# Optimization experiments

Measured on AMD Instinct MI355X. Metric: run time of the kernel, lower is better.

The kernel has to match this reference:

```python
import jax, jax.numpy as jnp
import numpy as np
from jax import lax

_F1 = np.array([1., 3., 3., 1.], dtype=np.float32)
_F1 = _F1 / _F1.sum()
F2D = jnp.asarray(np.outer(_F1, _F1))  # [4,4] normalized FIR filter
LRELU_GAIN = float(np.sqrt(2.0))


def _upfirdn2d_up(x, up, pad0, pad1, gain):
    # zero-insertion upsample + pad + FIR filter (VALID depthwise conv)
    B, C, H, W = x.shape
    if up > 1:
        x = jnp.zeros((B, C, H, up, W, up), x.dtype).at[:, :, :, 0, :, 0].set(x)
        x = x.reshape(B, C, H * up, W * up)
    x = jnp.pad(x, ((0, 0), (0, 0), (pad0, pad1), (pad0, pad1)))
    k = jnp.broadcast_to((F2D * gain).astype(x.dtype), (C, 1, 4, 4))
    return lax.conv_general_dilated(x, k, (1, 1), 'VALID', feature_group_count=C)


def _affine(w, aw, ab):
    # FullyConnectedLayer: weight_gain = 1/sqrt(in_features), bias_init handled in setup
    return w @ aw.T * (1.0 / np.sqrt(aw.shape[1])) + ab


def _mod_conv(x, weight, styles, up):
    # fused modulated conv2d with demodulation, batch-as-groups trick
    B = x.shape[0]
    O, I, kh, kw = weight.shape
    w = weight[None] * styles[:, None, :, None, None]          # [B,O,I,kh,kw]
    d = lax.rsqrt(jnp.sum(jnp.square(w), axis=(2, 3, 4)) + 1e-8)  # [B,O]
    w = w * d[:, :, None, None, None]
    if up == 2:
        # conv2d_resample: FIR upsample (gain=up^2), then true conv (flipped weight)
        # padding=1, fw=4, up=2 -> px0 = 1 + (4+2-1)//2 = 3, px1 = 1 + (4-2)//2 = 2
        x = _upfirdn2d_up(x, 2, 3, 2, 4.0)
        w = w[:, :, :, ::-1, ::-1]
        pad = 'VALID'
    else:
        pad = ((kh // 2, kh // 2), (kw // 2, kw // 2))
    xr = x.reshape(1, B * I, x.shape[2], x.shape[3])
    wr = w.reshape(B * O, I, kh, kw)
    y = lax.conv_general_dilated(xr, wr, (1, 1), pad, feature_group_count=B)
    return y.reshape(B, O, y.shape[2], y.shape[3])


def _lrelu_bias(x, b, clamp=256.0):
    # bias_act: lrelu(x+b) * sqrt(2), clamp
    x = x + b[None, :, None, None]
    x = jnp.where(x >= 0, x, 0.2 * x) * LRELU_GAIN
    return jnp.clip(x, -clamp, clamp)


def setup_inputs() -> dict:
    key = jax.random.key(0)
    ks = jax.random.split(key, 12)
    B, Cin, Cout, Wd, R, IC = 8, 512, 512, 512, 64, 3
    r = R // 2
    return dict(
        x=jax.random.normal(ks[0], (B, Cin, r, r), jnp.float32),
        img=jax.random.normal(ks[1], (B, IC, r, r), jnp.float32),
        ws=jax.random.normal(ks[2], (B, 3, Wd), jnp.float32),
        a0_w=jax.random.normal(ks[3], (Cin, Wd), jnp.float32),
        a0_b=jnp.ones((Cin,), jnp.float32),
        w0=jax.random.normal(ks[4], (Cout, Cin, 3, 3), jnp.float32),
        b0=jnp.zeros((Cout,), jnp.float32),
        ns0=jnp.asarray(0.1, jnp.float32),
        nc0=jax.random.normal(ks[5], (R, R), jnp.float32),
        a1_w=jax.random.normal(ks[6], (Cout, Wd), jnp.float32),
        a1_b=jnp.ones((Cout,), jnp.float32),
        w1=jax.random.normal(ks[7], (Cout, Cout, 3, 3), jnp.float32),
        b1=jnp.zeros((Cout,), jnp.float32),
        ns1=jnp.asarray(0.1, jnp.float32),
        nc1=jax.random.normal(ks[8], (R, R), jnp.float32),
        at_w=jax.random.normal(ks[9], (Cout, Wd), jnp.float32),
        at_b=jnp.ones((Cout,), jnp.float32),
        wt=jax.random.normal(ks[10], (IC, Cout), jnp.float32),
        bt=jnp.zeros((IC,), jnp.float32),
    )


def reference(x, img, ws, a0_w, a0_b, w0, b0, ns0, nc0,
              a1_w, a1_b, w1, b1, ns1, nc1, at_w, at_b, wt, bt):
    # conv0: modulated conv, up=2, const noise, lrelu bias-act with clamp
    s0 = _affine(ws[:, 0], a0_w, a0_b)
    h = _mod_conv(x, w0, s0, up=2)
    h = h + nc0[None, None] * ns0
    h = _lrelu_bias(h, b0)
    # conv1: modulated conv, up=1
    s1 = _affine(ws[:, 1], a1_w, a1_b)
    h = _mod_conv(h, w1, s1, up=1)
    h = h + nc1[None, None] * ns1
    h = _lrelu_bias(h, b1)
    # skip architecture: upsample img (upsample2d: px0=2, px1=1, gain=4)
    img_up = _upfirdn2d_up(img, 2, 2, 1, 4.0)
    # torgb: 1x1 modulated conv, no demodulation, styles scaled by weight_gain
    st = _affine(ws[:, 2], at_w, at_b) * (1.0 / np.sqrt(wt.shape[1]))
    y = jnp.einsum('bihw,bi,oi->bohw', h, st, wt)
    y = jnp.clip(y + bt[None, :, None, None], -256.0, 256.0)
    return h, img_up + y
```

## Files before the change

kernel.cpp:

```cpp
#include <hip/hip_runtime.h>
#include <stdint.h>

typedef unsigned short u16;
typedef unsigned int   u32;

#define DEVINL __device__ __forceinline__

typedef __bf16 bf16x8 __attribute__((ext_vector_type(8)));
typedef float  f32x4  __attribute__((ext_vector_type(4)));
typedef unsigned short u16x8 __attribute__((ext_vector_type(8)));

#define RSQRT512 0.044194173824159216f
#define LRELU_G  1.4142135623730951f

DEVINL u16 f2bf(float f) {
  union { float f; u32 u; } v; v.f = f;
  u32 r = v.u + 0x7fffu + ((v.u >> 16) & 1u);
  return (u16)(r >> 16);
}
DEVINL float bf2f(u16 b) {
  union { u32 u; float f; } v; v.u = ((u32)b) << 16;
  return v.f;
}

#define AS1 __attribute__((address_space(1)))
#define AS3 __attribute__((address_space(3)))
DEVINL void gload16(const void* g, void* l) {
  __builtin_amdgcn_global_load_lds((AS1 const u32*)(uintptr_t)g,
                                   (AS3 u32*)(u32)(uintptr_t)l, 16, 0, 0);
}

__global__ __launch_bounds__(256)
void style_kernel(const float* __restrict__ wsin,
                  const float* __restrict__ a0w, const float* __restrict__ a0b,
                  const float* __restrict__ a1w, const float* __restrict__ a1b,
                  const float* __restrict__ atw, const float* __restrict__ atb,
                  float* __restrict__ s_all)
{
  int wid = threadIdx.x >> 6, lane = threadIdx.x & 63;
  int idx = blockIdx.x * 4 + wid;
  int j = idx >> 12;
  int b = (idx >> 9) & 7;
  int o = idx & 511;
  const float* A  = (j == 0) ? a0w : ((j == 1) ? a1w : atw);
  const float* Ab = (j == 0) ? a0b : ((j == 1) ? a1b : atb);
  const float* wv = wsin + (b * 3 + j) * 512;
  float p = 0.f;
  #pragma unroll
  for (int m = 0; m < 512; m += 64) p += wv[m + lane] * A[(size_t)o * 512 + m + lane];
  #pragma unroll
  for (int s = 32; s; s >>= 1) p += __shfl_xor(p, s, 64);
  if (lane == 0) {
    float v = p * RSQRT512 + Ab[o];
    if (j == 2) v *= RSQRT512;
    s_all[idx] = v;
  }
}

__global__ __launch_bounds__(256)
void demod_kernel(const float* __restrict__ w, const float* __restrict__ s_j,
                  float* __restrict__ dOut)
{
  int b = blockIdx.x >> 9;
  int o = blockIdx.x & 511;
  __shared__ float s_sh[512];
  __shared__ float red[4];
  int t = threadIdx.x;
  s_sh[t]       = s_j[b * 512 + t];
  s_sh[t + 256] = s_j[b * 512 + t + 256];
  __syncthreads();
  float ssq = 0.f;
  #pragma unroll
  for (int hh = 0; hh < 2; ++hh) {
    int i = t + hh * 256;
    float si = s_sh[i];
    const float* wp = w + ((size_t)o * 512 + i) * 9;
    #pragma unroll
    for (int k = 0; k < 9; ++k) { float v = wp[k] * si; ssq += v * v; }
  }
  #pragma unroll
  for (int s = 32; s; s >>= 1) ssq += __shfl_xor(ssq, s, 64);
  if ((t & 63) == 0) red[t >> 6] = ssq;
  __syncthreads();
  if (t == 0) {
    float d = red[0] + red[1] + red[2] + red[3];
    dOut[b * 512 + o] = 1.0f / sqrtf(d + 1e-8f);
  }
}

template <int FLIP>
__global__ __launch_bounds__(256)
void wpack_kernel(const float* __restrict__ w, const float* __restrict__ s_j,
                  const float* __restrict__ dIn, u16* __restrict__ wg)
{
  int b = blockIdx.x >> 6;
  int kq = blockIdx.x & 63;
  float sv[8];
  #pragma unroll
  for (int e = 0; e < 8; ++e) sv[e] = s_j[b * 512 + kq * 8 + e];
  int t = threadIdx.x;
  #pragma unroll 1
  for (int rep = 0; rep < 2; ++rep) {
    int o = rep * 256 + t;
    float d = dIn[b * 512 + o];
    const float* wp = w + ((size_t)o * 512 + kq * 8) * 9;
    float wv[72];
    #pragma unroll
    for (int j = 0; j < 72; ++j) wv[j] = wp[j];
    #pragma unroll
    for (int tapOut = 0; tapOut < 9; ++tapOut) {
      int ksrc = FLIP ? (8 - tapOut) : tapOut;
      u16x8 g;
      #pragma unroll
      for (int e = 0; e < 8; ++e) g[e] = f2bf(wv[e * 9 + ksrc] * sv[e] * d);
      *(u16x8*)&wg[((((size_t)(b * 9 + tapOut)) * 64 + kq) * 512 + o) * 8] = g;
    }
  }
}

__global__ __launch_bounds__(256)
void upblur_kernel(const float* __restrict__ x, u16* __restrict__ xb)
{
  int b = blockIdx.x >> 6, c8 = blockIdx.x & 63;
  __shared__ float slab[8192];
  int t = threadIdx.x;
  const float* sp = x + (((size_t)(b * 512 + c8 * 8)) << 10);
  #pragma unroll
  for (int i = 0; i < 32; ++i) slab[t + i * 256] = sp[t + i * 256];
  __syncthreads();
  u16* ob = xb + ((size_t)(b * 64 + c8)) * 34848;
  #pragma unroll 1
  for (int idx = t; idx < 4356; idx += 256) {
    int p = idx / 66;
    int q = idx - p * 66;
    int m0, m1; float wy0, wy1;
    if ((p & 1) == 0) { m0 = (p >> 1) - 1; wy0 = 0.75f; m1 = p >> 1;       wy1 = 0.25f; }
    else              { m0 = (p - 3) >> 1; wy0 = 0.25f; m1 = (p - 1) >> 1; wy1 = 0.75f; }
    int n0, n1; float wx0, wx1;
    if ((q & 1) == 0) { n0 = (q >> 1) - 1; wx0 = 0.75f; n1 = q >> 1;       wx1 = 0.25f; }
    else              { n0 = (q - 3) >> 1; wx0 = 0.25f; n1 = (q - 1) >> 1; wx1 = 0.75f; }
    bool vm0 = (unsigned)m0 < 32u, vm1 = (unsigned)m1 < 32u;
    bool vn0 = (unsigned)n0 < 32u, vn1 = (unsigned)n1 < 32u;
    float w00 = (vm0 & vn0) ? wy0 * wx0 : 0.f;
    float w01 = (vm0 & vn1) ? wy0 * wx1 : 0.f;
    float w10 = (vm1 & vn0) ? wy1 * wx0 : 0.f;
    float w11 = (vm1 & vn1) ? wy1 * wx1 : 0.f;
    int i00 = ((m0 & 31) << 5) + (n0 & 31);
    int i01 = ((m0 & 31) << 5) + (n1 & 31);
    int i10 = ((m1 & 31) << 5) + (n0 & 31);
    int i11 = ((m1 & 31) << 5) + (n1 & 31);
    u16x8 g;
    #pragma unroll
    for (int e = 0; e < 8; ++e) {
      const float* se = slab + (e << 10);
      float a = w00 * se[i00] + w01 * se[i01] + w10 * se[i10] + w11 * se[i11];
      g[e] = f2bf(a);
    }
    *(u16x8*)&ob[idx * 8] = g;
  }
}

extern __shared__ u16 dynLds[];

template <int EPI>
__global__ __launch_bounds__(512, 2)
void conv8(const u16* __restrict__ xin,
           const u16* __restrict__ wg,
           const float* __restrict__ noise,
           const float* __restrict__ nsp,
           const float* __restrict__ bias,
           u16* __restrict__ hpOut,
           float* __restrict__ hOut)
{
  int blk = (blockIdx.x & 7) * 32 + (blockIdx.x >> 3);
  int b  = blk >> 5;
  int ot = (blk >> 4) & 1;
  int pt = blk & 15;
  int o0 = ot << 8;
  int y0 = pt << 2;

  int t = threadIdx.x;
  int w = t >> 6;
  int lane = t & 63;
  int gq = lane >> 4, r = lane & 15;
  int wm = w >> 2;
  int wn = w & 3;

  u16* Wb0 = dynLds;
  u16* Wb1 = dynLds + 16384;
  u16* Xb0 = dynLds + 32768;
  u16* Xb1 = dynLds + 49152;

  f32x4 acc[8][4];
  #pragma unroll
  for (int i = 0; i < 8; ++i)
    #pragma unroll
    for (int j = 0; j < 4; ++j) acc[i][j] = (f32x4){0.f, 0.f, 0.f, 0.f};

  const u16* wbB = wg + (size_t)b * 2359296;
  const u16* xbB = xin + (size_t)b * 2230272;

  auto STAGE = [&](int tile, int pb) {
    int tap = tile >> 3;
    int ck  = tile & 7;
    int dy = (tap * 171) >> 9;
    int dx = tap - dy * 3;
    u16* dW = (pb ? Wb1 : Wb0) + w * 2048;
    u16* dX = (pb ? Xb1 : Xb0) + w * 2048;
    const u16* wsrc = wbB + ((size_t)(tap * 64 + ck * 8 + w)) * 4096 + (size_t)o0 * 8;
    const u16* xsrc = xbB + ((size_t)(ck * 8 + w) * 66) * 66 * 8;
    #pragma unroll
    for (int q = 0; q < 4; ++q) {
      int row = q * 64 + lane;
      gload16(wsrc + (size_t)row * 8, dW + q * 512);
      int yy = y0 + q + dy;
      int xx = lane + dx;
      gload16(xsrc + (((size_t)yy * 66) + xx) * 8, dX + q * 512);
    }
  };

  auto TILE = [&](int pb) {
    const u16* Wp = pb ? Wb1 : Wb0;
    const u16* Xp = pb ? Xb1 : Xb0;
    const u16* A = (EPI == 0) ? Xp : Wp;
    const u16* B = (EPI == 0) ? Wp : Xp;
    bf16x8 bfr[4][2];
    #pragma unroll
    for (int fb = 0; fb < 4; ++fb)
      #pragma unroll
      for (int kk = 0; kk < 2; ++kk)
        bfr[fb][kk] = *(const bf16x8*)&B[((kk * 4 + gq) << 11) + ((wn * 64 + fb * 16 + r) << 3)];
    __builtin_amdgcn_s_setprio(1);
    #pragma unroll
    for (int fa = 0; fa < 8; ++fa) {
      int rowA = (wm * 128 + fa * 16 + r) << 3;
      bf16x8 a0 = *(const bf16x8*)&A[(gq << 11) + rowA];
      bf16x8 a1 = *(const bf16x8*)&A[((4 + gq) << 11) + rowA];
      #pragma unroll
      for (int fb = 0; fb < 4; ++fb) {
        acc[fa][fb] = __builtin_amdgcn_mfma_f32_16x16x32_bf16(a0, bfr[fb][0], acc[fa][fb], 0, 0, 0);
        acc[fa][fb] = __builtin_amdgcn_mfma_f32_16x16x32_bf16(a1, bfr[fb][1], acc[fa][fb], 0, 0, 0);
      }
    }
    __builtin_amdgcn_s_setprio(0);
  };

  STAGE(0, 0);
  STAGE(1, 1);
  asm volatile("s_waitcnt vmcnt(8)" ::: "memory");
  __builtin_amdgcn_sched_barrier(0);
  __builtin_amdgcn_s_barrier();
  __builtin_amdgcn_sched_barrier(0);

  int p = 0;
  #pragma unroll 1
  for (int tl = 0; tl < 72; ++tl) {
    TILE(p);
    __builtin_amdgcn_sched_barrier(0);
    __builtin_amdgcn_s_barrier();
    __builtin_amdgcn_sched_barrier(0);
    if (tl < 70) {
      STAGE(tl + 2, p);
      asm volatile("s_waitcnt vmcnt(8)" ::: "memory");
    } else if (tl == 70) {
      asm volatile("s_waitcnt vmcnt(0)" ::: "memory");
    }
    __builtin_amdgcn_sched_barrier(0);
    __builtin_amdgcn_s_barrier();
    __builtin_amdgcn_sched_barrier(0);
    p ^= 1;
  }
  __builtin_amdgcn_sched_barrier(0);

  float ns = nsp[0];
  if constexpr (EPI == 0) {
    #pragma unroll
    for (int fa = 0; fa < 8; ++fa) {
      #pragma unroll
      for (int fb = 0; fb < 4; ++fb) {
        int oo = o0 + wn * 64 + fb * 16 + r;
        float bo = bias[oo];
        #pragma unroll
        for (int v = 0; v < 4; ++v) {
          int px = wm * 128 + fa * 16 + gq * 4 + v;
          int pg = (pt << 8) + px;
          int y = pg >> 6, x2 = pg & 63;
          float val = acc[fa][fb][v] + noise[pg] * ns + bo;
          val = (val >= 0.f ? val : 0.2f * val) * LRELU_G;
          val = fminf(fmaxf(val, -256.f), 256.f);
          hpOut[((((size_t)b * 64 + (oo >> 3)) * 66 + (y + 1)) * 66 + (x2 + 1)) * 8 + (oo & 7)] = f2bf(val);
        }
      }
    }
  } else {
    #pragma unroll
    for (int fa = 0; fa < 8; ++fa) {
      #pragma unroll
      for (int fb = 0; fb < 4; ++fb) {
        int px = wn * 64 + fb * 16 + r;
        int pg = (pt << 8) + px;
        float nv = noise[pg] * ns;
        #pragma unroll
        for (int v = 0; v < 4; ++v) {
          int oo = o0 + wm * 128 + fa * 16 + gq * 4 + v;
          float val = acc[fa][fb][v] + nv + bias[oo];
          val = (val >= 0.f ? val : 0.2f * val) * LRELU_G;
          val = fminf(fmaxf(val, -256.f), 256.f);
          hOut[((size_t)(b * 512 + oo) << 12) + pg] = val;
        }
      }
    }
  }
}

__global__ __launch_bounds__(256)
void torgb_kernel(const float* __restrict__ h, const float* __restrict__ s_all,
                  const float* __restrict__ wt, const float* __restrict__ bt,
                  const float* __restrict__ img, float* __restrict__ out2)
{
  int b = blockIdx.x >> 4;
  int y = ((blockIdx.x & 15) << 2) + (threadIdx.x >> 6);
  int x = threadIdx.x & 63;
  __shared__ float stw[3][512];
  const float* st = s_all + 2 * 4096 + b * 512;
  for (int i = threadIdx.x; i < 512; i += 256) {
    float s = st[i];
    stw[0][i] = s * wt[i];
    stw[1][i] = s * wt[512 + i];
    stw[2][i] = s * wt[1024 + i];
  }
  __syncthreads();
  const float* hp = h + ((size_t)b * 512 << 12) + (y << 6) + x;
  float a0 = 0.f, a1 = 0.f, a2 = 0.f;
  #pragma unroll 8
  for (int i = 0; i < 512; ++i) {
    float v = hp[(size_t)i << 12];
    a0 += v * stw[0][i]; a1 += v * stw[1][i]; a2 += v * stw[2][i];
  }
  float accs[3] = {a0, a1, a2};
  int my0, my1; float wy0, wy1;
  if ((y & 1) == 0) { my0 = (y >> 1) - 1; wy0 = 0.25f; my1 = y >> 1;       wy1 = 0.75f; }
  else              { my0 = y >> 1;       wy0 = 0.75f; my1 = (y >> 1) + 1; wy1 = 0.25f; }
  int mx0, mx1; float wx0, wx1;
  if ((x & 1) == 0) { mx0 = (x >> 1) - 1; wx0 = 0.25f; mx1 = x >> 1;       wx1 = 0.75f; }
  else              { mx0 = x >> 1;       wx0 = 0.75f; mx1 = (x >> 1) + 1; wx1 = 0.25f; }
  bool vy0 = (unsigned)my0 < 32u, vy1 = (unsigned)my1 < 32u;
  bool vx0 = (unsigned)mx0 < 32u, vx1 = (unsigned)mx1 < 32u;
  #pragma unroll
  for (int o = 0; o < 3; ++o) {
    float yv = fminf(fmaxf(accs[o] + bt[o], -256.f), 256.f);
    const float* ib = img + ((size_t)(b * 3 + o) << 10);
    float iu = 0.f;
    if (vy0 & vx0) iu += wy0 * wx0 * ib[(my0 << 5) + mx0];
    if (vy0 & vx1) iu += wy0 * wx1 * ib[(my0 << 5) + mx1];
    if (vy1 & vx0) iu += wy1 * wx0 * ib[(my1 << 5) + mx0];
    if (vy1 & vx1) iu += wy1 * wx1 * ib[(my1 << 5) + mx1];
    out2[((size_t)(b * 3 + o) << 12) + (y << 6) + x] = iu + yv;
  }
}

extern "C" void kernel_launch(void* const* d_in, const int* in_sizes, int n_in,
                              void* d_out, int out_size, void* d_ws, size_t ws_size,
                              hipStream_t stream) {
  (void)in_sizes; (void)n_in; (void)out_size; (void)ws_size;
  const float* x   = (const float*)d_in[0];
  const float* img = (const float*)d_in[1];
  const float* ws_ = (const float*)d_in[2];
  const float* a0w = (const float*)d_in[3];
  const float* a0b = (const float*)d_in[4];
  const float* w0  = (const float*)d_in[5];
  const float* b0  = (const float*)d_in[6];
  const float* ns0 = (const float*)d_in[7];
  const float* nc0 = (const float*)d_in[8];
  const float* a1w = (const float*)d_in[9];
  const float* a1b = (const float*)d_in[10];
  const float* w1  = (const float*)d_in[11];
  const float* b1  = (const float*)d_in[12];
  const float* ns1 = (const float*)d_in[13];
  const float* nc1 = (const float*)d_in[14];
  const float* atw = (const float*)d_in[15];
  const float* atb = (const float*)d_in[16];
  const float* wt  = (const float*)d_in[17];
  const float* bt  = (const float*)d_in[18];

  char* wsp = (char*)d_ws;
  float* s_all = (float*)wsp;
  u16* wg0 = (u16*)(wsp + 49152);
  u16* wg1 = (u16*)(wsp + 49152 + 37748736ull);
  u16* xb  = (u16*)(wsp + 49152 + 2ull * 37748736);
  u16* hp  = (u16*)(wsp + 49152 + 2ull * 37748736 + 35684352);
  float* d0 = (float*)(wsp + 49152 + 2ull * 37748736 + 2ull * 35684352);
  float* d1 = (float*)(wsp + 49152 + 2ull * 37748736 + 2ull * 35684352 + 16384);

  float* h_out = (float*)d_out;
  float* out2  = (float*)d_out + 16777216;

  (void)hipFuncSetAttribute((const void*)conv8<0>,
                            hipFuncAttributeMaxDynamicSharedMemorySize, 131072);
  (void)hipFuncSetAttribute((const void*)conv8<1>,
                            hipFuncAttributeMaxDynamicSharedMemorySize, 131072);

  style_kernel<<<3072, 256, 0, stream>>>(ws_, a0w, a0b, a1w, a1b, atw, atb, s_all);
  demod_kernel<<<4096, 256, 0, stream>>>(w0, s_all, d0);
  demod_kernel<<<4096, 256, 0, stream>>>(w1, s_all + 4096, d1);
  wpack_kernel<1><<<512, 256, 0, stream>>>(w0, s_all, d0, wg0);
  wpack_kernel<0><<<512, 256, 0, stream>>>(w1, s_all + 4096, d1, wg1);
  upblur_kernel<<<512, 256, 0, stream>>>(x, xb);
  (void)hipMemsetAsync(hp, 0, 35684352, stream);
  conv8<0><<<256, 512, 131072, stream>>>(xb, wg0, nc0, ns0, b0, hp, nullptr);
  conv8<1><<<256, 512, 131072, stream>>>(hp, wg1, nc1, ns1, b1, nullptr, h_out);
  torgb_kernel<<<128, 256, 0, stream>>>(h_out, s_all, wt, bt, img, out2);
}
```

Before: 381.4 us.

## Split conv main loop into half-K phases interleaving staging with MFMA

Restructures the implicit-GEMM conv main loop into four phases per K tile, each covering half of K and half of the A fragments. Global-to-LDS loads for the next tile are issued in half-tile chunks between phases, with finer vmcnt waits and barriers, so memory traffic overlaps compute at a finer grain. The cost is more barriers per tile and tighter dependence on correct wait counts; the LDS layout is reorganized per half and per wave.

```diff
diff --git a/kernel.cpp b/kernel.cpp
--- a/kernel.cpp
+++ b/kernel.cpp
@@ -186,10 +186,10 @@
   int wm = w >> 2;
   int wn = w & 3;
 
-  u16* Wb0 = dynLds;
-  u16* Wb1 = dynLds + 16384;
-  u16* Xb0 = dynLds + 32768;
-  u16* Xb1 = dynLds + 49152;
+  u16* Wl = dynLds;
+  u16* Xl = dynLds + 32768;
+  const u16* Al = (EPI == 0) ? Xl : Wl;
+  const u16* Bl = (EPI == 0) ? Wl : Xl;
 
   f32x4 acc[8][4];
   #pragma unroll
@@ -200,77 +200,75 @@
   const u16* wbB = wg + (size_t)b * 2359296;
   const u16* xbB = xin + (size_t)b * 2230272;
 
-  auto STAGE = [&](int tile, int pb) {
+  int jl = w & 3;
+  int rb = w >> 2;
+
+  auto STAGEH = [&](int tile, int h) {
     int tap = tile >> 3;
     int ck  = tile & 7;
     int dy = (tap * 171) >> 9;
     int dx = tap - dy * 3;
-    u16* dW = (pb ? Wb1 : Wb0) + w * 2048;
-    u16* dX = (pb ? Xb1 : Xb0) + w * 2048;
-    const u16* wsrc = wbB + ((size_t)(tap * 64 + ck * 8 + w)) * 4096 + (size_t)o0 * 8;
-    const u16* xsrc = xbB + ((size_t)(ck * 8 + w) * 66) * 66 * 8;
-    #pragma unroll
-    for (int q = 0; q < 4; ++q) {
-      int row = q * 64 + lane;
-      gload16(wsrc + (size_t)row * 8, dW + q * 512);
-      int yy = y0 + q + dy;
-      int xx = lane + dx;
-      gload16(xsrc + (((size_t)yy * 66) + xx) * 8, dX + q * 512);
+    int jg = h * 4 + jl;
+    u32 base = (u32)((tile & 1) * 16384 + h * 8192 + jl * 2048 + rb * 1024);
+    const u16* wsrc = wbB + ((size_t)(tap * 64 + ck * 8 + jg)) * 4096
+                          + ((size_t)o0 + rb * 128) * 8;
+    const u16* xsrc = xbB + (size_t)(ck * 8 + jg) * 34848;
+    #pragma unroll
+    for (int q = 0; q < 2; ++q) {
+      gload16(wsrc + (size_t)(q * 64 + lane) * 8, Wl + base + q * 512);
+      int yy = y0 + rb * 2 + q + dy;
+      gload16(xsrc + (((size_t)yy * 66) + dx + lane) * 8, Xl + base + q * 512);
     }
   };
 
-  auto TILE = [&](int pb) {
-    const u16* Wp = pb ? Wb1 : Wb0;
-    const u16* Xp = pb ? Xb1 : Xb0;
-    const u16* A = (EPI == 0) ? Xp : Wp;
-    const u16* B = (EPI == 0) ? Wp : Xp;
-    bf16x8 bfr[4][2];
-    #pragma unroll
-    for (int fb = 0; fb < 4; ++fb)
+  auto PHASE = [&](int tb, int h, int faBase, bf16x8* bfr, bool readB,
+                   int stTile, int stH, int vm) {
+    u32 hb = (u32)(tb * 16384 + h * 8192) + ((u32)gq << 11);
+    if (readB) {
       #pragma unroll
-      for (int kk = 0; kk < 2; ++kk)
-        bfr[fb][kk] = *(const bf16x8*)&B[((kk * 4 + gq) << 11) + ((wn * 64 + fb * 16 + r) << 3)];
+      for (int fb = 0; fb < 4; ++fb)
+        bfr[fb] = *(const bf16x8*)&Bl[hb + ((wn * 64 + fb * 16 + r) << 3)];
+    }
+    bf16x8 af[4];
+    #pragma unroll
+    for (int i = 0; i < 4; ++i)
+      af[i] = *(const bf16x8*)&Al[hb + ((wm * 128 + (faBase + i) * 16 + r) << 3)];
+    if (stTile >= 0) STAGEH(stTile, stH);
+    if (vm == 4)      asm volatile("s_waitcnt vmcnt(4)" ::: "memory");
+    else if (vm == 0) asm volatile("s_waitcnt vmcnt(0)" ::: "memory");
+    __builtin_amdgcn_sched_barrier(0);
+    __builtin_amdgcn_s_barrier();
+    asm volatile("s_waitcnt lgkmcnt(0)" ::: "memory");
+    __builtin_amdgcn_sched_barrier(0);
     __builtin_amdgcn_s_setprio(1);
     #pragma unroll
-    for (int fa = 0; fa < 8; ++fa) {
-      int rowA = (wm * 128 + fa * 16 + r) << 3;
-      bf16x8 a0 = *(const bf16x8*)&A[(gq << 11) + rowA];
-      bf16x8 a1 = *(const bf16x8*)&A[((4 + gq) << 11) + rowA];
+    for (int i = 0; i < 4; ++i)
       #pragma unroll
-      for (int fb = 0; fb < 4; ++fb) {
-        acc[fa][fb] = __builtin_amdgcn_mfma_f32_16x16x32_bf16(a0, bfr[fb][0], acc[fa][fb], 0, 0, 0);
-        acc[fa][fb] = __builtin_amdgcn_mfma_f32_16x16x32_bf16(a1, bfr[fb][1], acc[fa][fb], 0, 0, 0);
-      }
-    }
+      for (int fb = 0; fb < 4; ++fb)
+        acc[faBase + i][fb] =
+            __builtin_amdgcn_mfma_f32_16x16x32_bf16(af[i], bfr[fb], acc[faBase + i][fb], 0, 0, 0);
     __builtin_amdgcn_s_setprio(0);
+    __builtin_amdgcn_sched_barrier(0);
+    __builtin_amdgcn_s_barrier();
   };
 
-  STAGE(0, 0);
-  STAGE(1, 1);
-  asm volatile("s_waitcnt vmcnt(8)" ::: "memory");
+  STAGEH(0, 0);
+  STAGEH(0, 1);
+  asm volatile("s_waitcnt vmcnt(4)" ::: "memory");
   __builtin_amdgcn_sched_barrier(0);
   __builtin_amdgcn_s_barrier();
-  __builtin_amdgcn_sched_barrier(0);
-
-  int p = 0;
+
   #pragma unroll 1
   for (int tl = 0; tl < 72; ++tl) {
-    TILE(p);
-    __builtin_amdgcn_sched_barrier(0);
-    __builtin_amdgcn_s_barrier();
-    __builtin_amdgcn_sched_barrier(0);
-    if (tl < 70) {
-      STAGE(tl + 2, p);
-      asm volatile("s_waitcnt vmcnt(8)" ::: "memory");
-    } else if (tl == 70) {
-      asm volatile("s_waitcnt vmcnt(0)" ::: "memory");
-    }
-    __builtin_amdgcn_sched_barrier(0);
-    __builtin_amdgcn_s_barrier();
-    __builtin_amdgcn_sched_barrier(0);
-    p ^= 1;
-  }
-  __builtin_amdgcn_sched_barrier(0);
+    int tb = tl & 1;
+    int nt = (tl < 71) ? tl + 1 : -1;
+    bf16x8 bfr0[4];
+    PHASE(tb, 0, 0, bfr0, true,  nt, 0, -1);
+    PHASE(tb, 0, 4, bfr0, false, -1, 0, (tl < 71) ? 4 : 0);
+    bf16x8 bfr1[4];
+    PHASE(tb, 1, 0, bfr1, true,  nt, 1, -1);
+    PHASE(tb, 1, 4, bfr1, false, -1, 0, (tl < 71) ? 4 : -1);
+  }
 
   float ns = nsp[0];
   if constexpr (EPI == 0) {
```

New measurement: 388.1 us. Within noise of the previous version (+1.8%).
